# Optimization experiments

Measured on AMD Instinct MI355X. Metric: run time of the kernel, lower is better.

Reference implementation:

```python
import jax, jax.numpy as jnp
import numpy as np

EPS_WHITEN = 1e-4
EPS_EIGH = 1e-6
LN_EPS = 1e-5
PROPER_ROT = True


def setup_inputs() -> dict:
    key = jax.random.key(0)
    ks = jax.random.split(key, 12)
    N, d, C, B = 131072, 4, 64, 1024
    std = 0.02
    return {
        "node_embeddings": jax.random.normal(ks[0], (N, d, C), jnp.float32),
        "batch": jnp.sort(jax.random.randint(ks[1], (N,), 0, B)),
        "num_graphs": B,
        "anchor": std * jax.random.normal(ks[2], (d, C), jnp.float32),
        "w1": std * jax.random.normal(ks[3], (C, C), jnp.float32),
        "b1": jnp.zeros((C,), jnp.float32),
        "w2": std * jax.random.normal(ks[4], (C, 1), jnp.float32),
        "b2": jnp.zeros((1,), jnp.float32),
        "token": std * jax.random.normal(ks[5], (1, d, C), jnp.float32),
        "wc1": std * jax.random.normal(ks[6], (2 * C, C), jnp.float32),
        "bc1": jnp.zeros((C,), jnp.float32),
        "wc2": std * jax.random.normal(ks[7], (C, C), jnp.float32),
        "bc2": jnp.zeros((C,), jnp.float32),
        "ln_g": jnp.ones((C,), jnp.float32),
        "ln_b": jnp.zeros((C,), jnp.float32),
    }


def _inv_sqrt_spd(S):
    # batched SPD inverse square root via eigh; S: [N, d, d]
    w, V = jnp.linalg.eigh(S)
    w = jnp.clip(w, EPS_EIGH)
    return jnp.einsum("nij,nj,nkj->nik", V, 1.0 / jnp.sqrt(w), V)


def _procrustes_align(Z, anchor):
    # find orthogonal R_i minimizing ||R_i Z_i - anchor||_F, return R_i Z_i
    M = jnp.einsum("dc,nec->nde", anchor, Z)  # [N, d, d]
    U, _, Vt = jnp.linalg.svd(M, full_matrices=False)
    if PROPER_ROT:
        det = jnp.linalg.det(jnp.einsum("nij,njk->nik", U, Vt))  # [N]
        U = U.at[:, :, -1].multiply(jnp.sign(det)[:, None])
    R = jnp.einsum("nij,njk->nik", U, Vt)
    return jnp.einsum("nij,njc->nic", R, Z)


def _layer_norm(x, g, b):
    mu = jnp.mean(x, axis=-1, keepdims=True)
    var = jnp.var(x, axis=-1, keepdims=True)
    return (x - mu) * jax.lax.rsqrt(var + LN_EPS) * g + b


def reference(node_embeddings, batch, num_graphs, anchor, w1, b1, w2, b2,
              token, wc1, bc1, wc2, bc2, ln_g, ln_b):
    H = node_embeddings  # [N, d, C]
    N, d, C = H.shape
    I = jnp.eye(d, dtype=H.dtype)
    S = jnp.einsum("ndc,nec->nde", H, H) + EPS_WHITEN * I  # [N, d, d]
    Z = jnp.einsum("nde,nec->ndc", _inv_sqrt_spd(S), H)    # whitened
    Z_aligned = _procrustes_align(Z, anchor)

    # invariant descriptor and per-node score
    u = jnp.sum(Z * Z, axis=1)                               # [N, C]
    h = jax.nn.gelu(u @ w1 + b1, approximate=False)
    scores = (h @ w2 + b2)[:, 0]                             # [N]

    # scatter softmax over graphs
    smax = jax.ops.segment_max(scores, batch, num_segments=num_graphs)
    e = jnp.exp(scores - smax[batch])
    denom = jax.ops.segment_sum(e, batch, num_segments=num_graphs)
    weights = e / denom[batch]                               # [N]

    pooled = jax.ops.segment_sum(Z_aligned * weights[:, None, None], batch,
                                 num_segments=num_graphs)    # [B, d, C]

    tok = jnp.broadcast_to(token, (num_graphs, d, C))
    combined = jnp.concatenate([tok, pooled], axis=-1)       # [B, d, 2C]
    hc = jax.nn.gelu(combined @ wc1 + bc1, approximate=False)
    updated = _layer_norm(hc @ wc2 + bc2, ln_g, ln_b)        # [B, d, C]
    return jnp.sum(updated * updated, axis=1)                # [B, C]
```

## Files before the change

kernel.cpp:

```cpp
#include <hip/hip_runtime.h>
#include <math.h>

#define WSG_STRIDE 260
#define ACC_STRIDE 257
#define MAXG 4
#define NPB 64

__device__ __forceinline__ float dot4f(float4 a, float4 b){
  return a.x*b.x + a.y*b.y + a.z*b.z + a.w*b.w;
}
__device__ __forceinline__ float gelu_exact(float x){
  return 0.5f*x*(1.0f+erff(x*0.70710678118654752440f));
}
__device__ __forceinline__ void mm44(float o[4][4], const float a[4][4], const float b[4][4]){
  #pragma unroll
  for (int i=0;i<4;++i){
    #pragma unroll
    for (int j=0;j<4;++j)
      o[i][j] = a[i][0]*b[0][j] + a[i][1]*b[1][j] + a[i][2]*b[2][j] + a[i][3]*b[3][j];
  }
}

template<int P,int Q,int K1,int K2>
__device__ __forceinline__ void jrot(float a[4][4], float V[4][4]){
  float apq = a[P][Q];
  if (fabsf(apq) > 1e-30f){
    float app=a[P][P], aqq=a[Q][Q];
    float tau=(aqq-app)/(2.0f*apq);
    float t=copysignf(1.0f,tau)/(fabsf(tau)+sqrtf(1.0f+tau*tau));
    float c=1.0f/sqrtf(1.0f+t*t), s=t*c;
    float a1p=a[K1][P], a1q=a[K1][Q];
    a[K1][P]=c*a1p-s*a1q; a[P][K1]=a[K1][P];
    a[K1][Q]=s*a1p+c*a1q; a[Q][K1]=a[K1][Q];
    float a2p=a[K2][P], a2q=a[K2][Q];
    a[K2][P]=c*a2p-s*a2q; a[P][K2]=a[K2][P];
    a[K2][Q]=s*a2p+c*a2q; a[Q][K2]=a[K2][Q];
    a[P][P]=app-t*apq; a[Q][Q]=aqq+t*apq; a[P][Q]=0.0f; a[Q][P]=0.0f;
    #pragma unroll
    for (int r=0;r<4;++r){ float vp=V[r][P], vq=V[r][Q]; V[r][P]=c*vp-s*vq; V[r][Q]=s*vp+c*vq; }
  }
}

__device__ __forceinline__ void jacobi4(float a[4][4], float V[4][4], int sweeps){
  #pragma unroll
  for (int i=0;i<4;++i){
    #pragma unroll
    for (int j=0;j<4;++j) V[i][j] = (i==j)?1.0f:0.0f;
  }
  for (int sw=0; sw<sweeps; ++sw){
    jrot<0,1,2,3>(a,V); jrot<0,2,1,3>(a,V); jrot<0,3,1,2>(a,V);
    jrot<1,2,0,3>(a,V); jrot<1,3,0,2>(a,V); jrot<2,3,0,1>(a,V);
  }
}

__device__ __forceinline__ float det4(const float V[4][4]){
  float s0 = V[0][0]*V[1][1] - V[0][1]*V[1][0];
  float s1 = V[0][0]*V[1][2] - V[0][2]*V[1][0];
  float s2 = V[0][0]*V[1][3] - V[0][3]*V[1][0];
  float s3 = V[0][1]*V[1][2] - V[0][2]*V[1][1];
  float s4 = V[0][1]*V[1][3] - V[0][3]*V[1][1];
  float s5 = V[0][2]*V[1][3] - V[0][3]*V[1][2];
  float c5 = V[2][2]*V[3][3] - V[2][3]*V[3][2];
  float c4 = V[2][1]*V[3][3] - V[2][3]*V[3][1];
  float c3 = V[2][1]*V[3][2] - V[2][2]*V[3][1];
  float c2 = V[2][0]*V[3][3] - V[2][3]*V[3][0];
  float c1 = V[2][0]*V[3][2] - V[2][2]*V[3][0];
  float c0 = V[2][0]*V[3][1] - V[2][1]*V[3][0];
  return s0*c5 - s1*c4 + s2*c3 + s3*c2 - s4*c1 + s5*c0;
}

__device__ __forceinline__ void phase2_body(const float Sd[10], const float Gd[16],
                                            float Wp[10], float Tout[16]){
  float a00=Sd[0]+1e-4f, a01=Sd[1], a02=Sd[2], a03=Sd[3];
  float a11=Sd[4]+1e-4f, a12=Sd[5], a13=Sd[6];
  float a22=Sd[7]+1e-4f, a23=Sd[8], a33=Sd[9]+1e-4f;
  float Gm[4][4];
  #pragma unroll
  for (int d=0;d<4;++d){
    #pragma unroll
    for (int f=0;f<4;++f) Gm[d][f]=Gd[4*d+f];
  }
  float cs = 0.4f*(a00+a11+a22+a33);
  float rc = 1.0f/cs;
  float Y[4][4], Z[4][4];
  Y[0][0]=a00*rc; Y[0][1]=Y[1][0]=a01*rc; Y[0][2]=Y[2][0]=a02*rc; Y[0][3]=Y[3][0]=a03*rc;
  Y[1][1]=a11*rc; Y[1][2]=Y[2][1]=a12*rc; Y[1][3]=Y[3][1]=a13*rc;
  Y[2][2]=a22*rc; Y[2][3]=Y[3][2]=a23*rc; Y[3][3]=a33*rc;
  #pragma unroll
  for (int i=0;i<4;++i){
    #pragma unroll
    for (int j=0;j<4;++j) Z[i][j]=(i==j)?1.0f:0.0f;
  }
  #pragma unroll
  for (int it=0; it<8; ++it){
    float P[4][4], Y2[4][4], Z2[4][4];
    mm44(P, Z, Y);
    #pragma unroll
    for (int i=0;i<4;++i){
      #pragma unroll
      for (int j=0;j<4;++j) P[i][j] = (i==j) ? 1.5f-0.5f*P[i][j] : -0.5f*P[i][j];
    }
    mm44(Y2, Y, P);
    mm44(Z2, P, Z);
    #pragma unroll
    for (int i=0;i<4;++i){
      #pragma unroll
      for (int j=0;j<4;++j){ Y[i][j]=Y2[i][j]; Z[i][j]=Z2[i][j]; }
    }
  }
  float rsc = rsqrtf(cs);
  float Wm[4][4];
  #pragma unroll
  for (int i=0;i<4;++i){
    #pragma unroll
    for (int j=0;j<4;++j) Wm[i][j] = Z[i][j]*rsc;
  }
  Wp[0]=Wm[0][0]; Wp[1]=Wm[0][1]; Wp[2]=Wm[0][2]; Wp[3]=Wm[0][3];
  Wp[4]=Wm[1][1]; Wp[5]=Wm[1][2]; Wp[6]=Wm[1][3];
  Wp[7]=Wm[2][2]; Wp[8]=Wm[2][3]; Wp[9]=Wm[3][3];
  float M[4][4];
  mm44(M, Gm, Wm);
  float A2[4][4];
  #pragma unroll
  for (int i=0;i<4;++i){
    #pragma unroll
    for (int j=0;j<4;++j)
      A2[i][j] = M[0][i]*M[0][j] + M[1][i]*M[1][j] + M[2][i]*M[2][j] + M[3][i]*M[3][j];
  }
  float V2[4][4];
  jacobi4(A2, V2, 4);
  float mu[4];
  #pragma unroll
  for (int i=0;i<4;++i) mu[i]=A2[i][i];
  #define CSW(I,J) if (mu[I] < mu[J]) { float tw; \
    tw=mu[I]; mu[I]=mu[J]; mu[J]=tw; \
    tw=V2[0][I]; V2[0][I]=V2[0][J]; V2[0][J]=tw; \
    tw=V2[1][I]; V2[1][I]=V2[1][J]; V2[1][J]=tw; \
    tw=V2[2][I]; V2[2][I]=V2[2][J]; V2[2][J]=tw; \
    tw=V2[3][I]; V2[3][I]=V2[3][J]; V2[3][J]=tw; }
  CSW(0,1) CSW(2,3) CSW(0,2) CSW(1,3) CSW(1,2)
  #undef CSW
  float u0[4],u1[4],u2[4];
  #pragma unroll
  for (int d=0;d<4;++d){
    u0[d]=M[d][0]*V2[0][0]+M[d][1]*V2[1][0]+M[d][2]*V2[2][0]+M[d][3]*V2[3][0];
    u1[d]=M[d][0]*V2[0][1]+M[d][1]*V2[1][1]+M[d][2]*V2[2][1]+M[d][3]*V2[3][1];
    u2[d]=M[d][0]*V2[0][2]+M[d][1]*V2[1][2]+M[d][2]*V2[2][2]+M[d][3]*V2[3][2];
  }
  {
    float dd = u0[0]*u0[0]+u0[1]*u0[1]+u0[2]*u0[2]+u0[3]*u0[3];
    float in0 = 1.0f/sqrtf(fmaxf(dd,1e-30f));
    #pragma unroll
    for (int d=0;d<4;++d) u0[d]*=in0;
    float p01 = u0[0]*u1[0]+u0[1]*u1[1]+u0[2]*u1[2]+u0[3]*u1[3];
    #pragma unroll
    for (int d=0;d<4;++d) u1[d]-=p01*u0[d];
    dd = u1[0]*u1[0]+u1[1]*u1[1]+u1[2]*u1[2]+u1[3]*u1[3];
    float in1 = 1.0f/sqrtf(fmaxf(dd,1e-30f));
    #pragma unroll
    for (int d=0;d<4;++d) u1[d]*=in1;
    float p02 = u0[0]*u2[0]+u0[1]*u2[1]+u0[2]*u2[2]+u0[3]*u2[3];
    float p12 = u1[0]*u2[0]+u1[1]*u2[1]+u1[2]*u2[2]+u1[3]*u2[3];
    #pragma unroll
    for (int d=0;d<4;++d) u2[d]-=p02*u0[d]+p12*u1[d];
    dd = u2[0]*u2[0]+u2[1]*u2[1]+u2[2]*u2[2]+u2[3]*u2[3];
    float in2 = 1.0f/sqrtf(fmaxf(dd,1e-30f));
    #pragma unroll
    for (int d=0;d<4;++d) u2[d]*=in2;
  }
  #define D3(p,q,r) (u0[p]*(u1[q]*u2[r]-u1[r]*u2[q]) - u1[p]*(u0[q]*u2[r]-u0[r]*u2[q]) + u2[p]*(u0[q]*u1[r]-u0[r]*u1[q]))
  float t3[4];
  t3[0] = -D3(1,2,3); t3[1] = D3(0,2,3); t3[2] = -D3(0,1,3); t3[3] = D3(0,1,2);
  #undef D3
  float dl = (det4(V2) >= 0.0f) ? 1.0f : -1.0f;
  float R[4][4];
  #pragma unroll
  for (int d=0;d<4;++d){
    #pragma unroll
    for (int e=0;e<4;++e)
      R[d][e] = u0[d]*V2[e][0] + u1[d]*V2[e][1] + u2[d]*V2[e][2] + dl*t3[d]*V2[e][3];
  }
  float Wr[4][4];
  Wr[0][0]=Wp[0]; Wr[0][1]=Wr[1][0]=Wp[1]; Wr[0][2]=Wr[2][0]=Wp[2]; Wr[0][3]=Wr[3][0]=Wp[3];
  Wr[1][1]=Wp[4]; Wr[1][2]=Wr[2][1]=Wp[5]; Wr[1][3]=Wr[3][1]=Wp[6];
  Wr[2][2]=Wp[7]; Wr[2][3]=Wr[3][2]=Wp[8]; Wr[3][3]=Wp[9];
  float T[4][4];
  mm44(T, R, Wr);
  #pragma unroll
  for (int d=0;d<4;++d){
    #pragma unroll
    for (int ee=0;ee<4;++ee) Tout[4*d+ee]=T[d][ee];
  }
}

#define PHASE1(HN, AL, SARR, GARR, IQ) { \
  _Pragma("unroll") \
  for (int j=0;j<4;++j){ \
    float4 h0 = *(const float4*)((HN) + 0*64 + j*16 + (IQ)*4); \
    float4 h1v= *(const float4*)((HN) + 1*64 + j*16 + (IQ)*4); \
    float4 h2 = *(const float4*)((HN) + 2*64 + j*16 + (IQ)*4); \
    float4 h3 = *(const float4*)((HN) + 3*64 + j*16 + (IQ)*4); \
    float4 a0 = *(const float4*)((AL) + 0*64 + j*16 + (IQ)*4); \
    float4 a1 = *(const float4*)((AL) + 1*64 + j*16 + (IQ)*4); \
    float4 a2 = *(const float4*)((AL) + 2*64 + j*16 + (IQ)*4); \
    float4 a3 = *(const float4*)((AL) + 3*64 + j*16 + (IQ)*4); \
    SARR[0]+=dot4f(h0,h0); SARR[1]+=dot4f(h0,h1v); SARR[2]+=dot4f(h0,h2); SARR[3]+=dot4f(h0,h3); \
    SARR[4]+=dot4f(h1v,h1v); SARR[5]+=dot4f(h1v,h2); SARR[6]+=dot4f(h1v,h3); \
    SARR[7]+=dot4f(h2,h2); SARR[8]+=dot4f(h2,h3); SARR[9]+=dot4f(h3,h3); \
    GARR[0]+=dot4f(a0,h0);  GARR[1]+=dot4f(a0,h1v);  GARR[2]+=dot4f(a0,h2);  GARR[3]+=dot4f(a0,h3); \
    GARR[4]+=dot4f(a1,h0);  GARR[5]+=dot4f(a1,h1v);  GARR[6]+=dot4f(a1,h2);  GARR[7]+=dot4f(a1,h3); \
    GARR[8]+=dot4f(a2,h0);  GARR[9]+=dot4f(a2,h1v);  GARR[10]+=dot4f(a2,h2); GARR[11]+=dot4f(a2,h3); \
    GARR[12]+=dot4f(a3,h0); GARR[13]+=dot4f(a3,h1v); GARR[14]+=dot4f(a3,h2); GARR[15]+=dot4f(a3,h3); \
  } }

#define ZPASS(ACCPTR, HNPTR, TMAT, EV, NQ, IQ) { \
  float* accp = (ACCPTR); \
  _Pragma("unroll") \
  for (int j=0;j<4;++j){ \
    float4 t0 = *(const float4*)((HNPTR) + 0*64 + j*16 + (IQ)*4); \
    float4 t1 = *(const float4*)((HNPTR) + 1*64 + j*16 + (IQ)*4); \
    float4 t2 = *(const float4*)((HNPTR) + 2*64 + j*16 + (IQ)*4); \
    float4 t3 = *(const float4*)((HNPTR) + 3*64 + j*16 + (IQ)*4); \
    float z0[4], z1[4], z2[4], z3[4]; \
    _Pragma("unroll") \
    for (int c=0;c<4;++c){ \
      float x0 = (c==0)?t0.x:(c==1)?t0.y:(c==2)?t0.z:t0.w; \
      float x1 = (c==0)?t1.x:(c==1)?t1.y:(c==2)?t1.z:t1.w; \
      float x2 = (c==0)?t2.x:(c==1)?t2.y:(c==2)?t2.z:t2.w; \
      float x3 = (c==0)?t3.x:(c==1)?t3.y:(c==2)?t3.z:t3.w; \
      z0[c] = TMAT[0][0]*x0+TMAT[0][1]*x1+TMAT[0][2]*x2+TMAT[0][3]*x3; \
      z1[c] = TMAT[1][0]*x0+TMAT[1][1]*x1+TMAT[1][2]*x2+TMAT[1][3]*x3; \
      z2[c] = TMAT[2][0]*x0+TMAT[2][1]*x1+TMAT[2][2]*x2+TMAT[2][3]*x3; \
      z3[c] = TMAT[3][0]*x0+TMAT[3][1]*x1+TMAT[3][2]*x2+TMAT[3][3]*x3; \
    } \
    _Pragma("unroll") \
    for (int dd=0;dd<4;++dd){ \
      int dsel = ((NQ) + dd) & 3; \
      _Pragma("unroll") \
      for (int c=0;c<4;++c){ \
        int csel = (((NQ)>>2) + c) & 3; \
        float zv = \
          (dsel==0)?((csel==0)?z0[0]:(csel==1)?z0[1]:(csel==2)?z0[2]:z0[3]): \
          (dsel==1)?((csel==0)?z1[0]:(csel==1)?z1[1]:(csel==2)?z1[2]:z1[3]): \
          (dsel==2)?((csel==0)?z2[0]:(csel==1)?z2[1]:(csel==2)?z2[2]:z2[3]): \
                    ((csel==0)?z3[0]:(csel==1)?z3[1]:(csel==2)?z3[2]:z3[3]); \
        atomicAdd(accp + dsel*64 + 16*j + 4*(IQ) + csel, (EV)*zv); \
      } \
    } \
  } }

#define SCORE_BODY(HN, WMAT, W1L, B1L, W2L, B2V, IQ, EOUT) { \
  float u[16]; \
  _Pragma("unroll") \
  for (int j=0;j<4;++j){ \
    float4 t0 = *(const float4*)((HN) + 0*64 + j*16 + (IQ)*4); \
    float4 t1 = *(const float4*)((HN) + 1*64 + j*16 + (IQ)*4); \
    float4 t2 = *(const float4*)((HN) + 2*64 + j*16 + (IQ)*4); \
    float4 t3 = *(const float4*)((HN) + 3*64 + j*16 + (IQ)*4); \
    _Pragma("unroll") \
    for (int c=0;c<4;++c){ \
      float x0 = (c==0)?t0.x:(c==1)?t0.y:(c==2)?t0.z:t0.w; \
      float x1 = (c==0)?t1.x:(c==1)?t1.y:(c==2)?t1.z:t1.w; \
      float x2 = (c==0)?t2.x:(c==1)?t2.y:(c==2)?t2.z:t2.w; \
      float x3 = (c==0)?t3.x:(c==1)?t3.y:(c==2)?t3.z:t3.w; \
      float w0 = WMAT[0][0]*x0+WMAT[0][1]*x1+WMAT[0][2]*x2+WMAT[0][3]*x3; \
      float w1v= WMAT[1][0]*x0+WMAT[1][1]*x1+WMAT[1][2]*x2+WMAT[1][3]*x3; \
      float w2v= WMAT[2][0]*x0+WMAT[2][1]*x1+WMAT[2][2]*x2+WMAT[2][3]*x3; \
      float w3 = WMAT[3][0]*x0+WMAT[3][1]*x1+WMAT[3][2]*x2+WMAT[3][3]*x3; \
      u[4*j+c] = w0*w0+w1v*w1v+w2v*w2v+w3*w3; \
    } \
  } \
  float h1[16]; \
  _Pragma("unroll") \
  for (int kk=0;kk<16;++kk) h1[kk]=B1L[(IQ)*16+kk]; \
  for (int m=0;m<4;++m){ \
    int qq = (IQ) ^ m; \
    _Pragma("unroll") \
    for (int jl=0;jl<16;++jl){ \
      float uu = __shfl_xor(u[jl], m); \
      int c = 16*(jl>>2) + 4*qq + (jl&3); \
      const float* wr = W1L + c*64 + (IQ)*16; \
      float4 wA=*(const float4*)(wr); \
      float4 wB=*(const float4*)(wr+4); \
      float4 wC=*(const float4*)(wr+8); \
      float4 wD=*(const float4*)(wr+12); \
      h1[0]+=uu*wA.x; h1[1]+=uu*wA.y; h1[2]+=uu*wA.z; h1[3]+=uu*wA.w; \
      h1[4]+=uu*wB.x; h1[5]+=uu*wB.y; h1[6]+=uu*wB.z; h1[7]+=uu*wB.w; \
      h1[8]+=uu*wC.x; h1[9]+=uu*wC.y; h1[10]+=uu*wC.z; h1[11]+=uu*wC.w; \
      h1[12]+=uu*wD.x; h1[13]+=uu*wD.y; h1[14]+=uu*wD.z; h1[15]+=uu*wD.w; \
    } \
  } \
  float sp = 0.0f; \
  _Pragma("unroll") \
  for (int kk=0;kk<16;++kk) sp += gelu_exact(h1[kk]) * W2L[(IQ)*16+kk]; \
  sp += __shfl_xor(sp,1); sp += __shfl_xor(sp,2); \
  EOUT = expf(sp + (B2V)); }


__global__ __launch_bounds__(256, 4) __attribute__((amdgpu_waves_per_eu(4,4)))
void sg_kernel(const float* __restrict__ H, const float* __restrict__ anchor,
               float* __restrict__ SGWT, int N)
{
  __shared__ float aL[256];
  const int tid = threadIdx.x;
  const int n0 = blockIdx.x * NPB;
  const int iq = tid & 3;
  const int nq = tid >> 2;
  aL[tid] = anchor[tid];
  __syncthreads();
  const int node = n0 + nq;
  if (node >= N) return;

  const float* Hn = H + (size_t)node*256;
  float S[10], G[16];
  #pragma unroll
  for (int r=0;r<10;++r) S[r]=0.0f;
  #pragma unroll
  for (int r=0;r<16;++r) G[r]=0.0f;
  PHASE1(Hn, aL, S, G, iq)
  #pragma unroll
  for (int r=0;r<10;++r){ S[r]+=__shfl_xor(S[r],1); S[r]+=__shfl_xor(S[r],2); }
  #pragma unroll
  for (int r=0;r<16;++r){ G[r]+=__shfl_xor(G[r],1); G[r]+=__shfl_xor(G[r],2); }
  if (iq==0){
    #pragma unroll
    for (int r=0;r<10;++r) SGWT[(size_t)r*N + node] = S[r];
    #pragma unroll
    for (int r=0;r<16;++r) SGWT[(size_t)(10+r)*N + node] = G[r];
  }
}

__global__ __launch_bounds__(256, 3) __attribute__((amdgpu_waves_per_eu(3,3)))
void svd_kernel(float* __restrict__ SGWT, int N)
{
  const int node = blockIdx.x*256 + threadIdx.x;
  if (node >= N) return;
  float Sd[10], Gd[16];
  #pragma unroll
  for (int r=0;r<10;++r) Sd[r]=SGWT[(size_t)r*N + node];
  #pragma unroll
  for (int r=0;r<16;++r) Gd[r]=SGWT[(size_t)(10+r)*N + node];
  float Wp[10], T[16];
  phase2_body(Sd, Gd, Wp, T);
  #pragma unroll
  for (int r=0;r<10;++r) SGWT[(size_t)r*N + node] = Wp[r];
  #pragma unroll
  for (int r=0;r<16;++r) SGWT[(size_t)(10+r)*N + node] = T[r];
}

__global__ __launch_bounds__(256, 4) __attribute__((amdgpu_waves_per_eu(4,4)))
void pool_kernel(
    const float* __restrict__ H, const int* __restrict__ batch,
    const float* __restrict__ SGWT, const float* __restrict__ w1g,
    const float* __restrict__ b1, const float* __restrict__ w2,
    const float* __restrict__ b2, float* __restrict__ wsAcc, int N)
{
  __shared__ float w1L[4096];
  __shared__ __align__(16) float TL[64*20];
  __shared__ float eL[64];
  __shared__ int   gL[64];
  __shared__ float b1L[64];
  __shared__ float w2L[64];

  const int tid = threadIdx.x;
  const int n0 = blockIdx.x * NPB;
  const int iq = tid & 3;
  const int nq = tid >> 2;

  for (int i=tid;i<4096;i+=256) w1L[i]=w1g[i];
  for (int i=tid;i<1024;i+=256){
    int nl = i & 63, r = i >> 6;
    int nd = n0 + nl;
    TL[nl*20 + r] = (nd < N) ? SGWT[(size_t)(10+r)*N + nd] : 0.0f;
  }
  if (tid < 64){
    int nd = n0 + tid;
    gL[tid] = batch[nd < N ? nd : (N-1)];
    eL[tid] = 0.0f;
    b1L[tid]=b1[tid]; w2L[tid]=w2[tid];
  }
  __syncthreads();

  const int node = n0 + nq;
  const bool valid = node < N;
  const float b2v = b2[0];

  if (valid){
    const float* Hn = H + (size_t)node*256;
    float Wq[10];
    #pragma unroll
    for (int r=0;r<10;++r) Wq[r]=SGWT[(size_t)r*N + node];
    float Wm[4][4];
    Wm[0][0]=Wq[0]; Wm[0][1]=Wm[1][0]=Wq[1]; Wm[0][2]=Wm[2][0]=Wq[2]; Wm[0][3]=Wm[3][0]=Wq[3];
    Wm[1][1]=Wq[4]; Wm[1][2]=Wm[2][1]=Wq[5]; Wm[1][3]=Wm[3][1]=Wq[6];
    Wm[2][2]=Wq[7]; Wm[2][3]=Wm[3][2]=Wq[8]; Wm[3][3]=Wq[9];
    float e;
    SCORE_BODY(Hn, Wm, w1L, b1L, w2L, b2v, iq, e)
    if (iq==0) eL[nq] = e;
  }
  __syncthreads();

  {
    const int c    = tid & 63;
    const int base = (tid >> 6) * 16;
    float a0=0.0f,a1=0.0f,a2=0.0f,a3=0.0f,aE=0.0f;
    int gcur = gL[base];
    for (int i=0;i<16;++i){
      int nl = base + i;
      int nd = n0 + nl;
      if (nd >= N) break;
      int g = gL[nl];
      if (g != gcur){
        float* wp = wsAcc + (size_t)gcur*WSG_STRIDE;
        atomicAdd(wp +        c, a0);
        atomicAdd(wp +  64 +  c, a1);
        atomicAdd(wp + 128 +  c, a2);
        atomicAdd(wp + 192 +  c, a3);
        if (c==0) atomicAdd(wp + 256, aE);
        a0=a1=a2=a3=aE=0.0f; gcur=g;
      }
      float e = eL[nl];
      const float* Hn2 = H + (size_t)nd*256;
      float h0 = Hn2[       c];
      float h1 = Hn2[ 64 +  c];
      float h2 = Hn2[128 +  c];
      float h3 = Hn2[192 +  c];
      const float* t = TL + nl*20;
      float4 T0 = *(const float4*)(t);
      float4 T1 = *(const float4*)(t+4);
      float4 T2 = *(const float4*)(t+8);
      float4 T3 = *(const float4*)(t+12);
      a0 += e*(T0.x*h0 + T0.y*h1 + T0.z*h2 + T0.w*h3);
      a1 += e*(T1.x*h0 + T1.y*h1 + T1.z*h2 + T1.w*h3);
      a2 += e*(T2.x*h0 + T2.y*h1 + T2.z*h2 + T2.w*h3);
      a3 += e*(T3.x*h0 + T3.y*h1 + T3.z*h2 + T3.w*h3);
      aE += e;
    }
    float* wp = wsAcc + (size_t)gcur*WSG_STRIDE;
    atomicAdd(wp +        c, a0);
    atomicAdd(wp +  64 +  c, a1);
    atomicAdd(wp + 128 +  c, a2);
    atomicAdd(wp + 192 +  c, a3);
    if (c==0) atomicAdd(wp + 256, aE);
  }
}

__global__ __launch_bounds__(256, 3) __attribute__((amdgpu_waves_per_eu(3,3)))
void node_kernel(
    const float* __restrict__ H, const int* __restrict__ batch,
    const float* __restrict__ anchor, const float* __restrict__ w1g,
    const float* __restrict__ b1, const float* __restrict__ w2,
    const float* __restrict__ b2, float* __restrict__ wsAcc, int N)
{
  __shared__ float w1L[4096];
  __shared__ float accL[MAXG*ACC_STRIDE];
  __shared__ float aL[256];
  __shared__ float b1L[64];
  __shared__ float w2L[64];

  const int tid = threadIdx.x;
  const int n0 = blockIdx.x * NPB;
  const int iq = tid & 3;
  const int nq = tid >> 2;
  const int lane = tid & 63;

  for (int i=tid;i<4096;i+=256) w1L[i]=w1g[i];
  aL[tid]=anchor[tid];
  if (tid < 64){ b1L[tid]=b1[tid]; w2L[tid]=w2[tid]; }
  for (int i=tid;i<MAXG*ACC_STRIDE;i+=256) accL[i]=0.0f;
  __syncthreads();

  const int node = n0 + nq;
  const bool valid = node < N;

  float S[10], G[16];
  #pragma unroll
  for (int r=0;r<10;++r) S[r]=0.0f;
  #pragma unroll
  for (int r=0;r<16;++r) G[r]=0.0f;
  if (valid){
    const float* Hn = H + (size_t)node*256;
    PHASE1(Hn, aL, S, G, iq)
  }
  #pragma unroll
  for (int r=0;r<10;++r){ S[r]+=__shfl_xor(S[r],1); S[r]+=__shfl_xor(S[r],2); }
  #pragma unroll
  for (int r=0;r<16;++r){ G[r]+=__shfl_xor(G[r],1); G[r]+=__shfl_xor(G[r],2); }

  const int srcOwn = (lane & 15) << 2;
  float Sd[10], Gd[16];
  #pragma unroll
  for (int r=0;r<10;++r) Sd[r]=__shfl(S[r], srcOwn);
  #pragma unroll
  for (int r=0;r<16;++r) Gd[r]=__shfl(G[r], srcOwn);

  float Wp[10], Tm[16];
  #pragma unroll
  for (int r=0;r<10;++r) Wp[r]=0.0f;
  #pragma unroll
  for (int r=0;r<16;++r) Tm[r]=0.0f;
  {
    const int node2 = n0 + ((tid>>6)<<4) + (lane & 15);
    if (lane < 16 && node2 < N){
      phase2_body(Sd, Gd, Wp, Tm);
    }
  }

  const float b2v = b2[0];
  const int gFirst = batch[n0];
  const int srcNode = lane >> 2;

  float Wq[10], Tq[16];
  #pragma unroll
  for (int r=0;r<10;++r) Wq[r]=__shfl(Wp[r], srcNode);
  #pragma unroll
  for (int r=0;r<16;++r) Tq[r]=__shfl(Tm[r], srcNode);

  if (valid){
    const float* Hn = H + (size_t)node*256;
    float Wm[4][4];
    Wm[0][0]=Wq[0]; Wm[0][1]=Wm[1][0]=Wq[1]; Wm[0][2]=Wm[2][0]=Wq[2]; Wm[0][3]=Wm[3][0]=Wq[3];
    Wm[1][1]=Wq[4]; Wm[1][2]=Wm[2][1]=Wq[5]; Wm[1][3]=Wm[3][1]=Wq[6];
    Wm[2][2]=Wq[7]; Wm[2][3]=Wm[3][2]=Wq[8]; Wm[3][3]=Wq[9];
    float e;
    SCORE_BODY(Hn, Wm, w1L, b1L, w2L, b2v, iq, e)

    asm volatile("" ::: "memory");
    float T[4][4];
    #pragma unroll
    for (int d=0;d<4;++d){
      #pragma unroll
      for (int e2=0;e2<4;++e2) T[d][e2]=Tq[4*d+e2];
    }
    int g  = batch[node];
    int gl = g - gFirst;
    if (gl < MAXG){
      ZPASS(accL + gl*ACC_STRIDE, Hn, T, e, nq, iq)
      if (iq==0) atomicAdd(accL + gl*ACC_STRIDE + 256, e);
    } else {
      ZPASS(wsAcc + (size_t)g*WSG_STRIDE, Hn, T, e, nq, iq)
      if (iq==0) atomicAdd(wsAcc + (size_t)g*WSG_STRIDE + 256, e);
    }
  }
  __syncthreads();

  {
    int lastIdx = n0+NPB-1 < N ? n0+NPB-1 : N-1;
    int gLast = batch[lastIdx];
    int ngl = gLast - gFirst + 1; if (ngl > MAXG) ngl = MAXG;
    for (int idx=tid; idx<ngl*ACC_STRIDE; idx+=256){
      int gl = idx / ACC_STRIDE;
      int sl = idx - gl*ACC_STRIDE;
      float v = accL[idx];
      if (v != 0.0f) atomicAdd(wsAcc + (size_t)(gFirst+gl)*WSG_STRIDE + sl, v);
    }
  }
}

__global__ __launch_bounds__(256) void finalize_kernel(
    const float* __restrict__ wsAcc, const float* __restrict__ token,
    const float* __restrict__ wc1, const float* __restrict__ bc1,
    const float* __restrict__ wc2, const float* __restrict__ bc2,
    const float* __restrict__ lng, const float* __restrict__ lnb,
    float* __restrict__ out)
{
  __shared__ float comb[4][128];
  __shared__ float hcL[4][64];
  __shared__ float upsq[4][64];
  const int g = blockIdx.x, tid = threadIdx.x;
  const int d = tid >> 6, k = tid & 63;
  const float* wsg = wsAcc + (size_t)g*WSG_STRIDE;
  float denom = wsg[256];
  float inv = (denom != 0.0f) ? 1.0f/denom : 0.0f;
  for (int i=tid;i<512;i+=256){
    int dd=i>>7, j=i&127;
    comb[dd][j] = (j<64) ? token[dd*64+j] : wsg[dd*64+(j-64)]*inv;
  }
  __syncthreads();
  float acc = bc1[k];
  for (int j=0;j<128;++j) acc += comb[d][j]*wc1[j*64+k];
  hcL[d][k] = gelu_exact(acc);
  __syncthreads();
  float acc2 = bc2[k];
  for (int j=0;j<64;++j) acc2 += hcL[d][j]*wc2[j*64+k];
  float s1 = acc2, s2 = acc2*acc2;
  #pragma unroll
  for (int m=1;m<64;m<<=1){ s1 += __shfl_xor(s1,m); s2 += __shfl_xor(s2,m); }
  float mu  = s1*(1.0f/64.0f);
  float var = s2*(1.0f/64.0f) - mu*mu;
  float up = (acc2 - mu)*(1.0f/sqrtf(var + 1e-5f))*lng[k] + lnb[k];
  upsq[d][k] = up*up;
  __syncthreads();
  if (tid < 64)
    out[(size_t)g*64 + tid] = upsq[0][tid]+upsq[1][tid]+upsq[2][tid]+upsq[3][tid];
}

extern "C" void kernel_launch(void* const* d_in, const int* in_sizes, int n_in,
                              void* d_out, int out_size, void* d_ws, size_t ws_size,
                              hipStream_t stream) {
  (void)n_in;
  const float* H      = (const float*)d_in[0];
  const int*   batch  = (const int*)  d_in[1];
  const float* anchor = (const float*)d_in[3];
  const float* w1     = (const float*)d_in[4];
  const float* b1     = (const float*)d_in[5];
  const float* w2     = (const float*)d_in[6];
  const float* b2     = (const float*)d_in[7];
  const float* token  = (const float*)d_in[8];
  const float* wc1    = (const float*)d_in[9];
  const float* bc1    = (const float*)d_in[10];
  const float* wc2    = (const float*)d_in[11];
  const float* bc2    = (const float*)d_in[12];
  const float* ln_g   = (const float*)d_in[13];
  const float* ln_b   = (const float*)d_in[14];
  float* out = (float*)d_out;

  const int N = in_sizes[0] / 256;
  const int B = out_size / 64;
  const int nb = (N + NPB - 1)/NPB;

  float* wsAcc = (float*)d_ws;
  const size_t needBase  = (size_t)B*WSG_STRIDE*sizeof(float);
  const size_t needSplit = needBase + (size_t)26*N*sizeof(float);

  hipMemsetAsync(wsAcc, 0, needBase, stream);

  if (ws_size >= needSplit){
    float* SGWT = wsAcc + (size_t)B*WSG_STRIDE;
    const int nsvd = (N + 255)/256;
    sg_kernel<<<nb, 256, 0, stream>>>(H, anchor, SGWT, N);
    svd_kernel<<<nsvd, 256, 0, stream>>>(SGWT, N);
    pool_kernel<<<nb, 256, 0, stream>>>(H, batch, SGWT, w1, b1, w2, b2, wsAcc, N);
  } else {
    node_kernel<<<nb, 256, 0, stream>>>(H, batch, anchor, w1, b1, w2, b2, wsAcc, N);
  }
  finalize_kernel<<<B, 256, 0, stream>>>(wsAcc, token, wc1, bc1, wc2, bc2, ln_g, ln_b, out);
}
```

Before: 314.1 us.

## Fuse Gram/cross-product and SVD kernels via shared-memory staging

```diff
diff --git a/kernel.cpp b/kernel.cpp
--- a/kernel.cpp
+++ b/kernel.cpp
@@ -5,6 +5,7 @@
 #define ACC_STRIDE 257
 #define MAXG 4
 #define NPB 64
+#define SG_STRIDE 27
 
 __device__ __forceinline__ float dot4f(float4 a, float4 b){
   return a.x*b.x + a.y*b.y + a.z*b.z + a.w*b.w;
@@ -298,54 +299,58 @@
 
 
 __global__ __launch_bounds__(256, 4) __attribute__((amdgpu_waves_per_eu(4,4)))
-void sg_kernel(const float* __restrict__ H, const float* __restrict__ anchor,
-               float* __restrict__ SGWT, int N)
+void sgsvd2_kernel(const float* __restrict__ H, const float* __restrict__ anchor,
+                   float* __restrict__ SGWT, int N)
 {
   __shared__ float aL[256];
+  __shared__ float sgL[256*SG_STRIDE];
   const int tid = threadIdx.x;
-  const int n0 = blockIdx.x * NPB;
+  const int n0 = blockIdx.x * 256;
   const int iq = tid & 3;
   const int nq = tid >> 2;
   aL[tid] = anchor[tid];
   __syncthreads();
-  const int node = n0 + nq;
-  if (node >= N) return;
-
-  const float* Hn = H + (size_t)node*256;
-  float S[10], G[16];
-  #pragma unroll
-  for (int r=0;r<10;++r) S[r]=0.0f;
-  #pragma unroll
-  for (int r=0;r<16;++r) G[r]=0.0f;
-  PHASE1(Hn, aL, S, G, iq)
-  #pragma unroll
-  for (int r=0;r<10;++r){ S[r]+=__shfl_xor(S[r],1); S[r]+=__shfl_xor(S[r],2); }
-  #pragma unroll
-  for (int r=0;r<16;++r){ G[r]+=__shfl_xor(G[r],1); G[r]+=__shfl_xor(G[r],2); }
-  if (iq==0){
-    #pragma unroll
-    for (int r=0;r<10;++r) SGWT[(size_t)r*N + node] = S[r];
-    #pragma unroll
-    for (int r=0;r<16;++r) SGWT[(size_t)(10+r)*N + node] = G[r];
-  }
-}
-
-__global__ __launch_bounds__(256, 3) __attribute__((amdgpu_waves_per_eu(3,3)))
-void svd_kernel(float* __restrict__ SGWT, int N)
-{
-  const int node = blockIdx.x*256 + threadIdx.x;
-  if (node >= N) return;
-  float Sd[10], Gd[16];
-  #pragma unroll
-  for (int r=0;r<10;++r) Sd[r]=SGWT[(size_t)r*N + node];
-  #pragma unroll
-  for (int r=0;r<16;++r) Gd[r]=SGWT[(size_t)(10+r)*N + node];
-  float Wp[10], T[16];
-  phase2_body(Sd, Gd, Wp, T);
-  #pragma unroll
-  for (int r=0;r<10;++r) SGWT[(size_t)r*N + node] = Wp[r];
-  #pragma unroll
-  for (int r=0;r<16;++r) SGWT[(size_t)(10+r)*N + node] = T[r];
+
+  for (int t=0;t<4;++t){
+    const int node = n0 + t*64 + nq;
+    float S[10], G[16];
+    #pragma unroll
+    for (int r=0;r<10;++r) S[r]=0.0f;
+    #pragma unroll
+    for (int r=0;r<16;++r) G[r]=0.0f;
+    if (node < N){
+      const float* Hn = H + (size_t)node*256;
+      PHASE1(Hn, aL, S, G, iq)
+    }
+    #pragma unroll
+    for (int r=0;r<10;++r){ S[r]+=__shfl_xor(S[r],1); S[r]+=__shfl_xor(S[r],2); }
+    #pragma unroll
+    for (int r=0;r<16;++r){ G[r]+=__shfl_xor(G[r],1); G[r]+=__shfl_xor(G[r],2); }
+    if (iq==0){
+      float* dst = sgL + (t*64 + nq)*SG_STRIDE;
+      #pragma unroll
+      for (int r=0;r<10;++r) dst[r]=S[r];
+      #pragma unroll
+      for (int r=0;r<16;++r) dst[10+r]=G[r];
+    }
+  }
+  __syncthreads();
+
+  const int node2 = n0 + tid;
+  if (node2 < N){
+    const float* src = sgL + tid*SG_STRIDE;
+    float Sd[10], Gd[16];
+    #pragma unroll
+    for (int r=0;r<10;++r) Sd[r]=src[r];
+    #pragma unroll
+    for (int r=0;r<16;++r) Gd[r]=src[10+r];
+    float Wp[10], T[16];
+    phase2_body(Sd, Gd, Wp, T);
+    #pragma unroll
+    for (int r=0;r<10;++r) SGWT[(size_t)r*N + node2] = Wp[r];
+    #pragma unroll
+    for (int r=0;r<16;++r) SGWT[(size_t)(10+r)*N + node2] = T[r];
+  }
 }
 
 __global__ __launch_bounds__(256, 4) __attribute__((amdgpu_waves_per_eu(4,4)))
@@ -627,9 +632,8 @@
 
   if (ws_size >= needSplit){
     float* SGWT = wsAcc + (size_t)B*WSG_STRIDE;
-    const int nsvd = (N + 255)/256;
-    sg_kernel<<<nb, 256, 0, stream>>>(H, anchor, SGWT, N);
-    svd_kernel<<<nsvd, 256, 0, stream>>>(SGWT, N);
+    const int nb2 = (N + 255)/256;
+    sgsvd2_kernel<<<nb2, 256, 0, stream>>>(H, anchor, SGWT, N);
     pool_kernel<<<nb, 256, 0, stream>>>(H, batch, SGWT, w1, b1, w2, b2, wsAcc, N);
   } else {
     node_kernel<<<nb, 256, 0, stream>>>(H, batch, anchor, w1, b1, w2, b2, wsAcc, N);
```

Measured after the change: 328.3 us. 4.5% more time.
